# Performance work log

Measured on AMD Instinct MI355X. Metric: run time of the kernel, lower is better.

## Reference

```python
import jax, jax.numpy as jnp
import numpy as np

B, E, P, L, D = 16, 2048, 16384, 5, 64  # batch, num_edges, num node-pairs, max_path_distance, edge_dim
EPS = 1e-9


def setup_inputs() -> dict:
    key = jax.random.key(0)
    k1, k2, k3 = jax.random.split(key, 3)
    edge_embedding = jax.random.normal(k1, (B, E, D), dtype=jnp.float32)
    # -1 marks padding (unused path slots), valid entries in [0, E)
    edge_paths = jax.random.randint(k2, (B, P, L), -1, E, dtype=jnp.int64)
    edge_vector = jax.random.normal(k3, (L, D), dtype=jnp.float32)
    return {"edge_embedding": edge_embedding, "edge_paths": edge_paths, "edge_vector": edge_vector}


def reference(edge_embedding, edge_paths, edge_vector):
    # edge_embedding: (B, E, D); edge_paths: (B, P, L) int with -1 padding; edge_vector: (L, D)
    edge_mask = edge_paths == -1                                     # (B, P, L)
    clamped = jnp.clip(edge_paths, 0, None)
    # batched gather: out[b, p, l, :] = edge_embedding[b, clamped[b, p, l], :]
    gathered = jax.vmap(lambda emb, idx: emb[idx])(edge_embedding, clamped)  # (B, P, L, D)
    gathered = jnp.where(edge_mask[..., None], jnp.zeros((), gathered.dtype), gathered)
    path_lengths = (~edge_mask).sum(axis=-1).astype(edge_embedding.dtype) + EPS  # (B, P)
    enc = jnp.einsum('beld,ld->be', gathered, edge_vector)           # (B, P)
    return enc / path_lengths
```

## Files before the change

### kernel.cpp

```cpp
#include <hip/hip_runtime.h>

#define B 16
#define E 2048
#define P 16384
#define L 5
#define D 64
#define EPS 1e-9f

__global__ __launch_bounds__(512) void edge_fused_kernel(
    const float* __restrict__ emb, const int* __restrict__ paths,
    const float* __restrict__ ev, float* __restrict__ out) {
    __shared__ float sev[L * D];
    __shared__ float sproj[E * L];

    const int t    = threadIdx.x;
    const int xcd  = blockIdx.x & 7;
    const int slot = blockIdx.x >> 3;
    const int b    = xcd * 2 + (slot & 1);
    const int g    = slot >> 1;

    int pidx[2][L];
    const int pbase = g * (P / 16);
#pragma unroll
    for (int k = 0; k < 2; ++k) {
        const int* pp = paths + ((size_t)b * P + pbase + k * 512 + t) * L;
#pragma unroll
        for (int l = 0; l < L; ++l) pidx[k][l] = pp[l];
    }

    for (int i = t; i < L * D; i += 512) sev[i] = ev[i];
    __syncthreads();

    const int half = t & 1;
    const int rt   = t >> 1;
    const float4* w4 = (const float4*)sev;
#pragma unroll
    for (int j = 0; j < E / 256; ++j) {
        const int e = rt + j * 256;
        const float4* src =
            (const float4*)(emb + ((size_t)b * E + e) * D + half * 32);
        float acc[L] = {0.f, 0.f, 0.f, 0.f, 0.f};
#pragma unroll
        for (int c = 0; c < 8; ++c) {
            float4 v = src[c];
#pragma unroll
            for (int l = 0; l < L; ++l) {
                float4 w = w4[l * 16 + half * 8 + c];
                acc[l] += v.x * w.x + v.y * w.y + v.z * w.z + v.w * w.w;
            }
        }
#pragma unroll
        for (int l = 0; l < L; ++l) acc[l] += __shfl_xor(acc[l], 1);
        if (half == 0) {
#pragma unroll
            for (int l = 0; l < L; ++l) sproj[e * L + l] = acc[l];
        }
    }
    __syncthreads();

#pragma unroll
    for (int k = 0; k < 2; ++k) {
        const int p = pbase + k * 512 + t;
        float sum = 0.f;
        int cnt = 0;
#pragma unroll
        for (int l = 0; l < L; ++l) {
            const int e = pidx[k][l];
            const bool valid = (e >= 0);
            const float v = sproj[(valid ? e : 0) * L + l];
            sum += valid ? v : 0.f;
            cnt += valid ? 1 : 0;
        }
        out[(size_t)b * P + p] = sum / ((float)cnt + EPS);
    }
}

extern "C" void kernel_launch(void* const* d_in, const int* in_sizes, int n_in,
                              void* d_out, int out_size, void* d_ws, size_t ws_size,
                              hipStream_t stream) {
    const float* emb   = (const float*)d_in[0];
    const int*   paths = (const int*)d_in[1];
    const float* ev    = (const float*)d_in[2];
    float* out = (float*)d_out;
    (void)d_ws; (void)ws_size;

    edge_fused_kernel<<<256, 512, 0, stream>>>(emb, paths, ev, out);
}
```

Before: 82.19 us.

## Split edge projection across grid with cooperative launch and grid sync

Previously each block recomputed the full per-batch edge projection, duplicating work 16 times per batch. Now every block projects a distinct slice of edge rows into a global workspace, the grid synchronizes via a cooperative launch, and each block then loads its batch's projections into shared memory for the path gather. This removes redundant embedding reads and dot products at the cost of a grid-wide barrier, a global round-trip for the projections, and cooperative-launch overhead.

```diff
diff --git a/kernel.cpp b/kernel.cpp
--- a/kernel.cpp
+++ b/kernel.cpp
@@ -1,4 +1,7 @@
 #include <hip/hip_runtime.h>
+#include <hip/hip_cooperative_groups.h>
+
+namespace cg = cooperative_groups;
 
 #define B 16
 #define E 2048
@@ -7,38 +10,35 @@
 #define D 64
 #define EPS 1e-9f
 
-__global__ __launch_bounds__(512) void edge_fused_kernel(
+__global__ __launch_bounds__(256) void edge_coop_kernel(
     const float* __restrict__ emb, const int* __restrict__ paths,
-    const float* __restrict__ ev, float* __restrict__ out) {
+    const float* __restrict__ ev, float* __restrict__ out,
+    float* __restrict__ proj) {
     __shared__ float sev[L * D];
     __shared__ float sproj[E * L];
 
-    const int t    = threadIdx.x;
-    const int xcd  = blockIdx.x & 7;
-    const int slot = blockIdx.x >> 3;
-    const int b    = xcd * 2 + (slot & 1);
-    const int g    = slot >> 1;
+    const int t = threadIdx.x;
+    const int b = blockIdx.x & 15;
+    const int g = blockIdx.x >> 4;
 
-    int pidx[2][L];
+    int pidx[4][L];
     const int pbase = g * (P / 16);
 #pragma unroll
-    for (int k = 0; k < 2; ++k) {
-        const int* pp = paths + ((size_t)b * P + pbase + k * 512 + t) * L;
+    for (int k = 0; k < 4; ++k) {
+        const int* pp = paths + ((size_t)b * P + pbase + k * 256 + t) * L;
 #pragma unroll
         for (int l = 0; l < L; ++l) pidx[k][l] = pp[l];
     }
 
-    for (int i = t; i < L * D; i += 512) sev[i] = ev[i];
+    for (int i = t; i < L * D; i += 256) sev[i] = ev[i];
     __syncthreads();
 
-    const int half = t & 1;
-    const int rt   = t >> 1;
-    const float4* w4 = (const float4*)sev;
-#pragma unroll
-    for (int j = 0; j < E / 256; ++j) {
-        const int e = rt + j * 256;
-        const float4* src =
-            (const float4*)(emb + ((size_t)b * E + e) * D + half * 32);
+    {
+        const int gid  = blockIdx.x * 256 + t;
+        const int row  = gid >> 1;
+        const int half = gid & 1;
+        const float4* src = (const float4*)(emb + (size_t)row * D + half * 32);
+        const float4* w4  = (const float4*)sev;
         float acc[L] = {0.f, 0.f, 0.f, 0.f, 0.f};
 #pragma unroll
         for (int c = 0; c < 8; ++c) {
@@ -52,26 +52,37 @@
 #pragma unroll
         for (int l = 0; l < L; ++l) acc[l] += __shfl_xor(acc[l], 1);
         if (half == 0) {
+            float* pr = proj + (size_t)row * L;
 #pragma unroll
-            for (int l = 0; l < L; ++l) sproj[e * L + l] = acc[l];
+            for (int l = 0; l < L; ++l) pr[l] = acc[l];
         }
     }
-    __syncthreads();
+
+    cg::this_grid().sync();
+
+    {
+        const float4* src = (const float4*)(proj + (size_t)b * E * L);
+        float4* dst = (float4*)sproj;
+#pragma unroll
+        for (int i = 0; i < (E * L) / 4 / 256; ++i)
+            dst[t + i * 256] = src[t + i * 256];
+        __syncthreads();
 
 #pragma unroll
-    for (int k = 0; k < 2; ++k) {
-        const int p = pbase + k * 512 + t;
-        float sum = 0.f;
-        int cnt = 0;
+        for (int k = 0; k < 4; ++k) {
+            const int p = pbase + k * 256 + t;
+            float sum = 0.f;
+            int cnt = 0;
 #pragma unroll
-        for (int l = 0; l < L; ++l) {
-            const int e = pidx[k][l];
-            const bool valid = (e >= 0);
-            const float v = sproj[(valid ? e : 0) * L + l];
-            sum += valid ? v : 0.f;
-            cnt += valid ? 1 : 0;
+            for (int l = 0; l < L; ++l) {
+                const int e = pidx[k][l];
+                const bool valid = (e >= 0);
+                const float v = sproj[(valid ? e : 0) * L + l];
+                sum += valid ? v : 0.f;
+                cnt += valid ? 1 : 0;
+            }
+            out[(size_t)b * P + p] = sum / ((float)cnt + EPS);
         }
-        out[(size_t)b * P + p] = sum / ((float)cnt + EPS);
     }
 }
 
@@ -81,8 +92,10 @@
     const float* emb   = (const float*)d_in[0];
     const int*   paths = (const int*)d_in[1];
     const float* ev    = (const float*)d_in[2];
-    float* out = (float*)d_out;
-    (void)d_ws; (void)ws_size;
+    float* out  = (float*)d_out;
+    float* proj = (float*)d_ws;
 
-    edge_fused_kernel<<<256, 512, 0, stream>>>(emb, paths, ev, out);
+    void* args[] = {(void*)&emb, (void*)&paths, (void*)&ev, (void*)&out, (void*)&proj};
+    hipLaunchCooperativeKernel((void*)edge_coop_kernel, dim3(B * P / 1024), dim3(256),
+                               args, 0, stream);
 }
```

Measured after the change: 100.7 us. 22.5% more time.

## Use fewer larger blocks with vectorized path loads and float4 output stores

Applied to the files above, without the earlier changes.

Cuts the grid from 256 blocks of 512 threads to 64 blocks of 1024 threads, so each block handles a quarter of a batch's node-pairs. The per-batch edge projection into shared memory is now recomputed 4 times per batch instead of 16. Path indices are loaded as contiguous int4 vectors, and each thread writes 4 outputs as one float4. The risk is that only 64 blocks cannot fill all compute units on the device, which may leave much of the GPU idle.

```diff
diff --git a/kernel.cpp b/kernel.cpp
--- a/kernel.cpp
+++ b/kernel.cpp
@@ -7,72 +7,79 @@
 #define D 64
 #define EPS 1e-9f
 
-__global__ __launch_bounds__(512) void edge_fused_kernel(
+__global__ __launch_bounds__(1024) void edge_fused4_kernel(
     const float* __restrict__ emb, const int* __restrict__ paths,
     const float* __restrict__ ev, float* __restrict__ out) {
     __shared__ float sev[L * D];
     __shared__ float sproj[E * L];
 
-    const int t    = threadIdx.x;
-    const int xcd  = blockIdx.x & 7;
-    const int slot = blockIdx.x >> 3;
-    const int b    = xcd * 2 + (slot & 1);
-    const int g    = slot >> 1;
+    const int t = threadIdx.x;
+    const int i = blockIdx.x;
+    const int b = (i & 7) + 8 * ((i >> 3) & 1);
+    const int g = i >> 4;
 
-    int pidx[2][L];
-    const int pbase = g * (P / 16);
+    const int4* pp = (const int4*)(paths + ((size_t)b * P + g * (P / 4)) * L);
+    int4 pv[5];
 #pragma unroll
-    for (int k = 0; k < 2; ++k) {
-        const int* pp = paths + ((size_t)b * P + pbase + k * 512 + t) * L;
-#pragma unroll
-        for (int l = 0; l < L; ++l) pidx[k][l] = pp[l];
-    }
+    for (int k = 0; k < 5; ++k) pv[k] = pp[t * 5 + k];
 
-    for (int i = t; i < L * D; i += 512) sev[i] = ev[i];
+    for (int idx = t; idx < L * D; idx += 1024) sev[idx] = ev[idx];
     __syncthreads();
 
-    const int half = t & 1;
-    const int rt   = t >> 1;
-    const float4* w4 = (const float4*)sev;
+    {
+        const int half = t & 1;
+        const int rbase = t >> 1;
+        const float4* w4 = (const float4*)sev;
 #pragma unroll
-    for (int j = 0; j < E / 256; ++j) {
-        const int e = rt + j * 256;
-        const float4* src =
-            (const float4*)(emb + ((size_t)b * E + e) * D + half * 32);
-        float acc[L] = {0.f, 0.f, 0.f, 0.f, 0.f};
+        for (int it = 0; it < 4; ++it) {
+            const int e = it * 512 + rbase;
+            const float4* src =
+                (const float4*)(emb + ((size_t)b * E + e) * D + half * 32);
+            float acc[L] = {0.f, 0.f, 0.f, 0.f, 0.f};
 #pragma unroll
-        for (int c = 0; c < 8; ++c) {
-            float4 v = src[c];
+            for (int c = 0; c < 8; ++c) {
+                float4 v = src[c];
 #pragma unroll
-            for (int l = 0; l < L; ++l) {
-                float4 w = w4[l * 16 + half * 8 + c];
-                acc[l] += v.x * w.x + v.y * w.y + v.z * w.z + v.w * w.w;
+                for (int l = 0; l < L; ++l) {
+                    float4 w = w4[l * 16 + half * 8 + c];
+                    acc[l] += v.x * w.x + v.y * w.y + v.z * w.z + v.w * w.w;
+                }
             }
-        }
 #pragma unroll
-        for (int l = 0; l < L; ++l) acc[l] += __shfl_xor(acc[l], 1);
-        if (half == 0) {
+            for (int l = 0; l < L; ++l) acc[l] += __shfl_xor(acc[l], 1);
+            if (half == 0) {
 #pragma unroll
-            for (int l = 0; l < L; ++l) sproj[e * L + l] = acc[l];
+                for (int l = 0; l < L; ++l) sproj[e * L + l] = acc[l];
+            }
         }
     }
     __syncthreads();
 
+    int pidx[20];
 #pragma unroll
-    for (int k = 0; k < 2; ++k) {
-        const int p = pbase + k * 512 + t;
+    for (int k = 0; k < 5; ++k) {
+        pidx[k * 4 + 0] = pv[k].x;
+        pidx[k * 4 + 1] = pv[k].y;
+        pidx[k * 4 + 2] = pv[k].z;
+        pidx[k * 4 + 3] = pv[k].w;
+    }
+    float4 res;
+    float* rp = (float*)&res;
+#pragma unroll
+    for (int k = 0; k < 4; ++k) {
         float sum = 0.f;
         int cnt = 0;
 #pragma unroll
         for (int l = 0; l < L; ++l) {
-            const int e = pidx[k][l];
+            const int e = pidx[k * 5 + l];
             const bool valid = (e >= 0);
             const float v = sproj[(valid ? e : 0) * L + l];
             sum += valid ? v : 0.f;
             cnt += valid ? 1 : 0;
         }
-        out[(size_t)b * P + p] = sum / ((float)cnt + EPS);
+        rp[k] = sum / ((float)cnt + EPS);
     }
+    *(float4*)(out + (size_t)b * P + g * (P / 4) + t * 4) = res;
 }
 
 extern "C" void kernel_launch(void* const* d_in, const int* in_sizes, int n_in,
@@ -84,5 +91,5 @@
     float* out = (float*)d_out;
     (void)d_ws; (void)ws_size;
 
-    edge_fused_kernel<<<256, 512, 0, stream>>>(emb, paths, ev, out);
+    edge_fused4_kernel<<<64, 1024, 0, stream>>>(emb, paths, ev, out);
 }
```

Result: no change. 81.52 us (-0.8%).
